# Optimization experiments

Measured on AMD Instinct MI355X. Metric: run time of the kernel, lower is better.

The kernel has to match this reference:

```python
import jax, jax.numpy as jnp
import numpy as np

NODE_IN, EDGE_IN, HID, L = 16, 8, 128, 4
N_NODES, N_EDGES = 50000, 600000
EPS = 1e-5


def setup_inputs() -> dict:
    key = jax.random.key(0)
    ks = jax.random.split(key, 20)
    def lin(k, fan_in, fan_out):
        b = 1.0 / np.sqrt(fan_in)
        kw, kb = jax.random.split(k)
        return (jax.random.uniform(kw, (fan_in, fan_out), jnp.float32, -b, b),
                jax.random.uniform(kb, (fan_out,), jnp.float32, -b, b))
    x = jax.random.normal(ks[0], (N_NODES, NODE_IN), jnp.float32)
    edge_index = jax.random.randint(ks[1], (2, N_EDGES), 0, N_NODES, jnp.int64)
    edge_attr = jax.random.normal(ks[2], (N_EDGES, EDGE_IN), jnp.float32)
    node_w, node_b = lin(ks[3], NODE_IN, HID)
    edge_w, edge_b = lin(ks[4], EDGE_IN, HID)
    lnode_w, lnode_b, ledge_w, ledge_b, adm_w, adm_b = [], [], [], [], [], []
    for l in range(L):
        w, b = lin(ks[5 + 3 * l], HID, HID); lnode_w.append(w); lnode_b.append(b)
        w, b = lin(ks[6 + 3 * l], HID, HID); ledge_w.append(w); ledge_b.append(b)
        w, b = lin(ks[7 + 3 * l], HID, 1); adm_w.append(w); adm_b.append(b)
    return {
        "x": x, "edge_index": edge_index, "edge_attr": edge_attr,
        "node_w": node_w, "node_b": node_b, "edge_w": edge_w, "edge_b": edge_b,
        "lnode_w": jnp.stack(lnode_w), "lnode_b": jnp.stack(lnode_b),
        "ledge_w": jnp.stack(ledge_w), "ledge_b": jnp.stack(ledge_b),
        "adm_w": jnp.stack(adm_w), "adm_b": jnp.stack(adm_b),
        "gamma": jnp.ones((L, HID), jnp.float32),
        "beta": jnp.zeros((L, HID), jnp.float32),
    }


def reference(x, edge_index, edge_attr, node_w, node_b, edge_w, edge_b,
              lnode_w, lnode_b, ledge_w, ledge_b, adm_w, adm_b, gamma, beta):
    N = x.shape[0]
    src, dst = edge_index[0], edge_index[1]
    h = x @ node_w + node_b              # [N, HID]
    ea = edge_attr @ edge_w + edge_b     # [E, HID]
    for l in range(lnode_w.shape[0]):
        hn = h @ lnode_w[l] + lnode_b[l]                         # lin_node
        y_mag = jax.nn.sigmoid(ea @ adm_w[l] + adm_b[l])         # [E, 1] admittance gate
        e = ea @ ledge_w[l] + ledge_b[l]                         # lin_edge
        msg = y_mag * (hn[src] + e)                              # gated message [E, HID]
        agg = jax.ops.segment_sum(msg, dst, num_segments=N)      # scatter-add
        mu = jnp.mean(agg, axis=-1, keepdims=True)
        var = jnp.mean((agg - mu) ** 2, axis=-1, keepdims=True)
        xn = (agg - mu) * jax.lax.rsqrt(var + EPS) * gamma[l] + beta[l]
        h = h + jax.nn.relu(xn)          # dropout is identity in eval mode
    return h
```

## Files before the change

kernel.cpp:

```cpp
#include <hip/hip_runtime.h>
#include <math.h>

#define N_NODES 50000
#define N_EDGES 600000
#define HID 128
#define NLAYERS 4
#define NODE_IN 16
#define EDGE_IN 8
#define LN_EPS 1e-5f
#define SCAN_BLOCKS ((N_NODES + 255) / 256)

typedef short bf16x8 __attribute__((ext_vector_type(8)));
typedef float f32x4 __attribute__((ext_vector_type(4)));

__device__ __forceinline__ float b2f(unsigned short u) {
    union { unsigned int i; float f; } v; v.i = ((unsigned int)u) << 16; return v.f;
}
__device__ __forceinline__ unsigned short f2b(float x) {
    union { float f; unsigned int i; } v; v.f = x;
    unsigned int b = v.i + 0x7FFFu + ((v.i >> 16) & 1u);
    return (unsigned short)(b >> 16);
}

__global__ void detect_i64(const int* ei, int* flag) {
    __shared__ int nz;
    if (threadIdx.x == 0) nz = 0;
    __syncthreads();
    int acc = 0;
    for (int i = threadIdx.x; i < 1024; i += blockDim.x)
        if (ei[2 * i + 1] != 0) acc = 1;
    if (acc) atomicOr(&nz, 1);
    __syncthreads();
    if (threadIdx.x == 0) *flag = (nz == 0) ? 1 : 0;
}

__device__ __forceinline__ int edge_src(const void* ei, int f, int e) {
    if (f) return (int)((const long long*)ei)[e];
    return ((const int*)ei)[e];
}
__device__ __forceinline__ int edge_dst(const void* ei, int f, int e) {
    if (f) return (int)((const long long*)ei)[N_EDGES + e];
    return ((const int*)ei)[N_EDGES + e];
}

__global__ void hist_k(const void* ei, const int* flag, int* cursor) {
    int e = blockIdx.x * blockDim.x + threadIdx.x;
    if (e >= N_EDGES) return;
    int f = *flag;
    atomicAdd(&cursor[edge_dst(ei, f, e)], 1);
}

__global__ void scan1_k(const int* __restrict__ cursor, int* __restrict__ locex,
                        int* __restrict__ partials) {
    __shared__ int sd[256];
    int t = threadIdx.x, i = blockIdx.x * 256 + t;
    int v = (i < N_NODES) ? cursor[i] : 0;
    sd[t] = v;
    __syncthreads();
    for (int off = 1; off < 256; off <<= 1) {
        int x = (t >= off) ? sd[t - off] : 0;
        __syncthreads();
        sd[t] += x;
        __syncthreads();
    }
    if (i < N_NODES) locex[i] = sd[t] - v;
    if (t == 255) partials[blockIdx.x] = sd[255];
}

__global__ void scan2_k(int* partials) {
    __shared__ int sd[256];
    int t = threadIdx.x;
    int v = (t < SCAN_BLOCKS) ? partials[t] : 0;
    sd[t] = v;
    __syncthreads();
    for (int off = 1; off < 256; off <<= 1) {
        int x = (t >= off) ? sd[t - off] : 0;
        __syncthreads();
        sd[t] += x;
        __syncthreads();
    }
    if (t < SCAN_BLOCKS) partials[t] = sd[t] - v;
    if (t == 255) partials[SCAN_BLOCKS] = sd[255];
}

__global__ void scan3_k(int* __restrict__ row_ptr, int* __restrict__ cursor,
                        const int* __restrict__ partials) {
    int i = blockIdx.x * 256 + threadIdx.x;
    if (i < N_NODES) {
        int r = row_ptr[i] + partials[blockIdx.x];
        row_ptr[i] = r;
        cursor[i] = r;
    }
    if (i == N_NODES) row_ptr[N_NODES] = partials[SCAN_BLOCKS];
}

__global__ void place_k(const void* ei, const int* flag, int* cursor,
                        int* sorted_src, int* sorted_eid) {
    int e = blockIdx.x * blockDim.x + threadIdx.x;
    if (e >= N_EDGES) return;
    int f = *flag;
    int s = edge_src(ei, f, e);
    int d = edge_dst(ei, f, e);
    int pos = atomicAdd(&cursor[d], 1);
    sorted_src[pos] = s;
    sorted_eid[pos] = e;
}

__global__ void precompute_k(const float* __restrict__ edge_w, const float* __restrict__ edge_b,
                             const float* __restrict__ ledge_w, const float* __restrict__ ledge_b,
                             const float* __restrict__ lnode_b,
                             const float* __restrict__ adm_w, const float* __restrict__ adm_b,
                             float* __restrict__ M, float* __restrict__ cb,
                             float* __restrict__ v, float* __restrict__ cgate) {
    int t = blockIdx.x * 256 + threadIdx.x;
    if (t < 4096) {
        int l = t >> 10, k = (t >> 7) & 7, ch = t & 127;
        const float* lw = ledge_w + (size_t)l * HID * HID;
        float a = 0.f;
        for (int j = 0; j < HID; ++j) a += edge_w[k * HID + j] * lw[j * HID + ch];
        M[t] = a;
    } else if (t < 4608) {
        int u = t - 4096;
        int l = u >> 7, ch = u & 127;
        const float* lw = ledge_w + (size_t)l * HID * HID;
        float a = ledge_b[l * HID + ch] + lnode_b[l * HID + ch];
        for (int j = 0; j < HID; ++j) a += edge_b[j] * lw[j * HID + ch];
        cb[u] = a;
    } else if (t < 4640) {
        int u = t - 4608;
        int l = u >> 3, k = u & 7;
        float a = 0.f;
        for (int j = 0; j < HID; ++j) a += edge_w[k * HID + j] * adm_w[l * HID + j];
        v[u] = a;
    } else if (t < 4644) {
        int l = t - 4640;
        float a = adm_b[l];
        for (int j = 0; j < HID; ++j) a += edge_b[j] * adm_w[l * HID + j];
        cgate[l] = a;
    }
}

__global__ void convertw_k(const float* __restrict__ lnode_w, unsigned short* __restrict__ Wt16) {
    int idx = blockIdx.x * 256 + threadIdx.x;
    if (idx >= NLAYERS * HID * HID) return;
    int l = idx >> 14, r = idx & 16383, n = r >> 7, k = r & 127;
    Wt16[idx] = f2b(lnode_w[(size_t)l * HID * HID + k * HID + n]);
}

__global__ __launch_bounds__(256) void reorder_k(
    const int* __restrict__ sorted_eid, const float* __restrict__ edge_attr,
    const float* __restrict__ vw, const float* __restrict__ cgate,
    float* __restrict__ ea_sorted, float* __restrict__ y_sorted) {
    __shared__ float sv[36];
    if (threadIdx.x < 32) sv[threadIdx.x] = vw[threadIdx.x];
    else if (threadIdx.x < 36) sv[threadIdx.x] = cgate[threadIdx.x - 32];
    __syncthreads();
    int p = blockIdx.x * 256 + threadIdx.x;
    if (p >= N_EDGES) return;
    int eid = sorted_eid[p];
    float4 a0 = ((const float4*)edge_attr)[(size_t)eid * 2];
    float4 a1 = ((const float4*)edge_attr)[(size_t)eid * 2 + 1];
    ((float4*)ea_sorted)[(size_t)p * 2] = a0;
    ((float4*)ea_sorted)[(size_t)p * 2 + 1] = a1;
#pragma unroll
    for (int l = 0; l < NLAYERS; ++l) {
        const float* vl = &sv[l * 8];
        float t = sv[32 + l];
        t += a0.x * vl[0] + a0.y * vl[1] + a0.z * vl[2] + a0.w * vl[3];
        t += a1.x * vl[4] + a1.y * vl[5] + a1.z * vl[6] + a1.w * vl[7];
        y_sorted[(size_t)l * N_EDGES + p] = 1.0f / (1.0f + __expf(-t));
    }
}

__global__ __launch_bounds__(256) void node_stats_k(
    const int* __restrict__ row_ptr, const float* __restrict__ ea_sorted,
    const float* __restrict__ y_sorted,
    float* __restrict__ agg8, float* __restrict__ sy_arr) {
    int lane = threadIdx.x & 63;
    int n = (blockIdx.x * 256 + threadIdx.x) >> 6;
    int es = lane >> 3, k = lane & 7;
    int ps = row_ptr[n], pe = row_ptr[n + 1];
    float a0 = 0.f, a1 = 0.f, a2 = 0.f, a3 = 0.f;
    float s0 = 0.f, s1 = 0.f, s2 = 0.f, s3 = 0.f;
    for (int p = ps + es; p < pe; p += 8) {
        float ea = ea_sorted[(size_t)p * EDGE_IN + k];
        float y0 = y_sorted[(size_t)0 * N_EDGES + p];
        float y1 = y_sorted[(size_t)1 * N_EDGES + p];
        float y2 = y_sorted[(size_t)2 * N_EDGES + p];
        float y3 = y_sorted[(size_t)3 * N_EDGES + p];
        a0 += y0 * ea; a1 += y1 * ea; a2 += y2 * ea; a3 += y3 * ea;
        s0 += y0; s1 += y1; s2 += y2; s3 += y3;
    }
#pragma unroll
    for (int m = 8; m <= 32; m <<= 1) {
        a0 += __shfl_xor(a0, m, 64); a1 += __shfl_xor(a1, m, 64);
        a2 += __shfl_xor(a2, m, 64); a3 += __shfl_xor(a3, m, 64);
        s0 += __shfl_xor(s0, m, 64); s1 += __shfl_xor(s1, m, 64);
        s2 += __shfl_xor(s2, m, 64); s3 += __shfl_xor(s3, m, 64);
    }
    if (lane < 8) {
        agg8[((size_t)0 * N_NODES + n) * 8 + k] = a0;
        agg8[((size_t)1 * N_NODES + n) * 8 + k] = a1;
        agg8[((size_t)2 * N_NODES + n) * 8 + k] = a2;
        agg8[((size_t)3 * N_NODES + n) * 8 + k] = a3;
    }
    if (lane == 0) {
        sy_arr[(size_t)0 * N_NODES + n] = s0;
        sy_arr[(size_t)1 * N_NODES + n] = s1;
        sy_arr[(size_t)2 * N_NODES + n] = s2;
        sy_arr[(size_t)3 * N_NODES + n] = s3;
    }
}

__global__ void node_encode_k(const float* __restrict__ x, const float* __restrict__ nw,
                              const float* __restrict__ nb, float* __restrict__ h,
                              unsigned short* __restrict__ h16) {
    int idx = blockIdx.x * 256 + threadIdx.x;
    if (idx >= N_NODES * HID) return;
    int n = idx >> 7, c = idx & 127;
    float acc = nb[c];
#pragma unroll
    for (int k = 0; k < NODE_IN; ++k) acc += x[n * NODE_IN + k] * nw[k * HID + c];
    h[idx] = acc;
    h16[idx] = f2b(acc);
}

__global__ __launch_bounds__(256) void gather16_k(
    const int* __restrict__ row_ptr, const int* __restrict__ sorted_src,
    const float* __restrict__ y_l, const unsigned short* __restrict__ h16,
    unsigned int* __restrict__ gh16) {
    int lane = threadIdx.x & 63;
    int n = (blockIdx.x * 256 + threadIdx.x) >> 6;
    int ps = row_ptr[n], pe = row_ptr[n + 1];
    float a0 = 0.f, a1 = 0.f;
    int p = ps;
    for (; p + 7 < pe; p += 8) {
        int s[8];
        float y[8];
        unsigned int v[8];
#pragma unroll
        for (int i = 0; i < 8; ++i) { s[i] = sorted_src[p + i]; y[i] = y_l[p + i]; }
#pragma unroll
        for (int i = 0; i < 8; ++i)
            v[i] = *(const unsigned int*)(h16 + (size_t)s[i] * HID + lane * 2);
#pragma unroll
        for (int i = 0; i < 8; ++i) {
            a0 += y[i] * b2f((unsigned short)v[i]);
            a1 += y[i] * b2f((unsigned short)(v[i] >> 16));
        }
    }
    for (; p + 3 < pe; p += 4) {
        int s[4];
        float y[4];
        unsigned int v[4];
#pragma unroll
        for (int i = 0; i < 4; ++i) { s[i] = sorted_src[p + i]; y[i] = y_l[p + i]; }
#pragma unroll
        for (int i = 0; i < 4; ++i)
            v[i] = *(const unsigned int*)(h16 + (size_t)s[i] * HID + lane * 2);
#pragma unroll
        for (int i = 0; i < 4; ++i) {
            a0 += y[i] * b2f((unsigned short)v[i]);
            a1 += y[i] * b2f((unsigned short)(v[i] >> 16));
        }
    }
    for (; p < pe; ++p) {
        float y = y_l[p];
        unsigned int v = *(const unsigned int*)(h16 + (size_t)sorted_src[p] * HID + lane * 2);
        a0 += y * b2f((unsigned short)v);
        a1 += y * b2f((unsigned short)(v >> 16));
    }
    gh16[(size_t)n * 64 + lane] = ((unsigned int)f2b(a1) << 16) | f2b(a0);
}

__global__ __launch_bounds__(256) void mfma_ln_k(
    const unsigned short* __restrict__ gh16, const unsigned short* __restrict__ Wt16,
    const float* __restrict__ M_l, const float* __restrict__ cb_l,
    const float* __restrict__ agg8_l, const float* __restrict__ sy_l,
    const float* __restrict__ gm, const float* __restrict__ bt,
    const float* __restrict__ h_in, float* __restrict__ h_out,
    unsigned short* __restrict__ h16_out) {
    __shared__ float red[4][16][2];
    const int tid = threadIdx.x;
    const int w = tid >> 6, lane = tid & 63;
    const int g = lane >> 4, c = lane & 15;
    const int nbase = blockIdx.x * 16;
    const int cf0 = w * 2;

    bf16x8 afrag[4];
#pragma unroll
    for (int kc = 0; kc < 4; ++kc)
        afrag[kc] = *(const bf16x8*)(gh16 + (size_t)(nbase + c) * HID + kc * 32 + g * 8);

    f32x4 acc[2];
#pragma unroll
    for (int t = 0; t < 2; ++t) {
        acc[t] = (f32x4){0.f, 0.f, 0.f, 0.f};
        const unsigned short* wp = Wt16 + (size_t)((cf0 + t) * 16 + c) * HID + g * 8;
#pragma unroll
        for (int kc = 0; kc < 4; ++kc) {
            bf16x8 bfrag = *(const bf16x8*)(wp + kc * 32);
            acc[t] = __builtin_amdgcn_mfma_f32_16x16x32_bf16(afrag[kc], bfrag, acc[t], 0, 0, 0);
        }
    }

    float cbv[2], gav[2], bev[2], mv[2][8];
#pragma unroll
    for (int t = 0; t < 2; ++t) {
        int ch = (cf0 + t) * 16 + c;
        cbv[t] = cb_l[ch]; gav[t] = gm[ch]; bev[t] = bt[ch];
#pragma unroll
        for (int k = 0; k < 8; ++k) mv[t][k] = M_l[k * HID + ch];
    }
#pragma unroll
    for (int r = 0; r < 4; ++r) {
        int node = nbase + 4 * g + r;
        float sy = sy_l[node];
        float4 t0 = ((const float4*)agg8_l)[(size_t)node * 2];
        float4 t1 = ((const float4*)agg8_l)[(size_t)node * 2 + 1];
        float a8[8] = {t0.x, t0.y, t0.z, t0.w, t1.x, t1.y, t1.z, t1.w};
#pragma unroll
        for (int t = 0; t < 2; ++t) {
            float v = sy * cbv[t];
#pragma unroll
            for (int k = 0; k < 8; ++k) v += a8[k] * mv[t][k];
            acc[t][r] += v;
        }
    }

    float sx[4], sq[4];
#pragma unroll
    for (int r = 0; r < 4; ++r) {
        sx[r] = acc[0][r] + acc[1][r];
        sq[r] = acc[0][r] * acc[0][r] + acc[1][r] * acc[1][r];
    }
#pragma unroll
    for (int m = 1; m <= 8; m <<= 1) {
#pragma unroll
        for (int r = 0; r < 4; ++r) {
            sx[r] += __shfl_xor(sx[r], m, 64);
            sq[r] += __shfl_xor(sq[r], m, 64);
        }
    }
    if (c == 0) {
#pragma unroll
        for (int r = 0; r < 4; ++r) {
            red[w][4 * g + r][0] = sx[r];
            red[w][4 * g + r][1] = sq[r];
        }
    }
    __syncthreads();

#pragma unroll
    for (int r = 0; r < 4; ++r) {
        int row = 4 * g + r;
        float SX = red[0][row][0] + red[1][row][0] + red[2][row][0] + red[3][row][0];
        float SQ = red[0][row][1] + red[1][row][1] + red[2][row][1] + red[3][row][1];
        float mean = SX * (1.0f / HID);
        float var = SQ * (1.0f / HID) - mean * mean;
        float rstd = rsqrtf(var + LN_EPS);
        int node = nbase + row;
#pragma unroll
        for (int t = 0; t < 2; ++t) {
            int ch = (cf0 + t) * 16 + c;
            float d = acc[t][r] - mean;
            float o = h_in[(size_t)node * HID + ch] +
                      fmaxf(d * rstd * gav[t] + bev[t], 0.f);
            h_out[(size_t)node * HID + ch] = o;
            h16_out[(size_t)node * HID + ch] = f2b(o);
        }
    }
}

extern "C" void kernel_launch(void* const* d_in, const int* in_sizes, int n_in,
                              void* d_out, int out_size, void* d_ws, size_t ws_size,
                              hipStream_t stream) {
    const float* x         = (const float*)d_in[0];
    const void*  ei        = d_in[1];
    const float* edge_attr = (const float*)d_in[2];
    const float* node_w    = (const float*)d_in[3];
    const float* node_b    = (const float*)d_in[4];
    const float* edge_w    = (const float*)d_in[5];
    const float* edge_b    = (const float*)d_in[6];
    const float* lnode_w   = (const float*)d_in[7];
    const float* lnode_b   = (const float*)d_in[8];
    const float* ledge_w   = (const float*)d_in[9];
    const float* ledge_b   = (const float*)d_in[10];
    const float* adm_w     = (const float*)d_in[11];
    const float* adm_b     = (const float*)d_in[12];
    const float* gamma     = (const float*)d_in[13];
    const float* beta      = (const float*)d_in[14];
    float* h = (float*)d_out;

    char* wp = (char*)d_ws;
    auto alloc = [&](size_t bytes) -> void* {
        void* p = (void*)wp;
        wp += (bytes + 255) & ~(size_t)255;
        return p;
    };
    int*            flag       = (int*)alloc(256);
    int*            cursor     = (int*)alloc(sizeof(int) * N_NODES);
    int*            row_ptr    = (int*)alloc(sizeof(int) * (N_NODES + 1));
    int*            partials   = (int*)alloc(sizeof(int) * (SCAN_BLOCKS + 1));
    int*            sorted_src = (int*)alloc(sizeof(int) * N_EDGES);
    int*            sorted_eid = (int*)alloc(sizeof(int) * N_EDGES);
    float*          ea_sorted  = (float*)alloc(sizeof(float) * (size_t)N_EDGES * EDGE_IN);
    float*          y_sorted   = (float*)alloc(sizeof(float) * NLAYERS * N_EDGES);
    float*          agg8       = (float*)alloc(sizeof(float) * NLAYERS * N_NODES * 8);
    float*          sy_arr     = (float*)alloc(sizeof(float) * NLAYERS * N_NODES);
    float*          Mw         = (float*)alloc(sizeof(float) * NLAYERS * 8 * HID);
    float*          cbw        = (float*)alloc(sizeof(float) * NLAYERS * HID);
    float*          vw         = (float*)alloc(sizeof(float) * NLAYERS * 8);
    float*          cgate      = (float*)alloc(sizeof(float) * NLAYERS);
    float*          hbuf       = (float*)alloc(sizeof(float) * (size_t)N_NODES * HID);
    unsigned short* h16        = (unsigned short*)alloc(sizeof(short) * (size_t)N_NODES * HID);
    unsigned short* gh16       = (unsigned short*)alloc(sizeof(short) * (size_t)N_NODES * HID);
    unsigned short* Wt16       = (unsigned short*)alloc(sizeof(short) * NLAYERS * HID * HID);
    (void)ws_size; (void)in_sizes; (void)n_in; (void)out_size;

    hipMemsetAsync(cursor, 0, sizeof(int) * N_NODES, stream);
    detect_i64<<<1, 256, 0, stream>>>((const int*)ei, flag);
    hist_k<<<(N_EDGES + 255) / 256, 256, 0, stream>>>(ei, flag, cursor);
    scan1_k<<<SCAN_BLOCKS, 256, 0, stream>>>(cursor, row_ptr, partials);
    scan2_k<<<1, 256, 0, stream>>>(partials);
    scan3_k<<<SCAN_BLOCKS, 256, 0, stream>>>(row_ptr, cursor, partials);
    place_k<<<(N_EDGES + 255) / 256, 256, 0, stream>>>(ei, flag, cursor, sorted_src, sorted_eid);
    precompute_k<<<19, 256, 0, stream>>>(edge_w, edge_b, ledge_w, ledge_b, lnode_b,
                                         adm_w, adm_b, Mw, cbw, vw, cgate);
    convertw_k<<<(NLAYERS * HID * HID + 255) / 256, 256, 0, stream>>>(lnode_w, Wt16);
    reorder_k<<<(N_EDGES + 255) / 256, 256, 0, stream>>>(sorted_eid, edge_attr,
                                                         vw, cgate, ea_sorted, y_sorted);
    node_stats_k<<<N_NODES / 4, 256, 0, stream>>>(row_ptr, ea_sorted, y_sorted,
                                                  agg8, sy_arr);
    node_encode_k<<<(N_NODES * HID + 255) / 256, 256, 0, stream>>>(x, node_w, node_b, h, h16);

    float* hin = h;
    float* hout = hbuf;
    for (int l = 0; l < NLAYERS; ++l) {
        gather16_k<<<N_NODES / 4, 256, 0, stream>>>(
            row_ptr, sorted_src, y_sorted + (size_t)l * N_EDGES, h16, (unsigned int*)gh16);
        mfma_ln_k<<<N_NODES / 16, 256, 0, stream>>>(
            gh16, Wt16 + (size_t)l * HID * HID,
            Mw + (size_t)l * 8 * HID, cbw + (size_t)l * HID,
            agg8 + (size_t)l * N_NODES * 8, sy_arr + (size_t)l * N_NODES,
            gamma + (size_t)l * HID, beta + (size_t)l * HID,
            hin, hout, h16);
        float* t = hin; hin = hout; hout = t;
    }
}
```

Measured before the change: 376.8 us.

## Apply node linear before gather and fuse gather with LayerNorm epilogue

```diff
diff --git a/kernel.cpp b/kernel.cpp
--- a/kernel.cpp
+++ b/kernel.cpp
@@ -225,10 +225,46 @@
     h16[idx] = f2b(acc);
 }
 
-__global__ __launch_bounds__(256) void gather16_k(
+__global__ __launch_bounds__(256) void mfma_hn_k(
+    const unsigned short* __restrict__ h16, const unsigned short* __restrict__ Wt16,
+    unsigned short* __restrict__ hn16) {
+    const int tid = threadIdx.x;
+    const int w = tid >> 6, lane = tid & 63;
+    const int g = lane >> 4, c = lane & 15;
+    const int nbase = blockIdx.x * 16;
+    const int cf0 = w * 2;
+
+    bf16x8 afrag[4];
+#pragma unroll
+    for (int kc = 0; kc < 4; ++kc)
+        afrag[kc] = *(const bf16x8*)(h16 + (size_t)(nbase + c) * HID + kc * 32 + g * 8);
+
+    f32x4 acc[2];
+#pragma unroll
+    for (int t = 0; t < 2; ++t) {
+        acc[t] = (f32x4){0.f, 0.f, 0.f, 0.f};
+        const unsigned short* wp = Wt16 + (size_t)((cf0 + t) * 16 + c) * HID + g * 8;
+#pragma unroll
+        for (int kc = 0; kc < 4; ++kc) {
+            bf16x8 bfrag = *(const bf16x8*)(wp + kc * 32);
+            acc[t] = __builtin_amdgcn_mfma_f32_16x16x32_bf16(afrag[kc], bfrag, acc[t], 0, 0, 0);
+        }
+    }
+#pragma unroll
+    for (int t = 0; t < 2; ++t)
+#pragma unroll
+        for (int r = 0; r < 4; ++r)
+            hn16[(size_t)(nbase + 4 * g + r) * HID + (cf0 + t) * 16 + c] = f2b(acc[t][r]);
+}
+
+__global__ __launch_bounds__(256) void gather_ln_k(
     const int* __restrict__ row_ptr, const int* __restrict__ sorted_src,
-    const float* __restrict__ y_l, const unsigned short* __restrict__ h16,
-    unsigned int* __restrict__ gh16) {
+    const float* __restrict__ y_l, const unsigned short* __restrict__ hn16,
+    const float* __restrict__ M_l, const float* __restrict__ cb_l,
+    const float* __restrict__ agg8_l, const float* __restrict__ sy_l,
+    const float* __restrict__ gm, const float* __restrict__ bt,
+    const float* __restrict__ h_in, float* __restrict__ h_out,
+    unsigned short* __restrict__ h16_out) {
     int lane = threadIdx.x & 63;
     int n = (blockIdx.x * 256 + threadIdx.x) >> 6;
     int ps = row_ptr[n], pe = row_ptr[n + 1];
@@ -242,7 +278,7 @@
         for (int i = 0; i < 8; ++i) { s[i] = sorted_src[p + i]; y[i] = y_l[p + i]; }
 #pragma unroll
         for (int i = 0; i < 8; ++i)
-            v[i] = *(const unsigned int*)(h16 + (size_t)s[i] * HID + lane * 2);
+            v[i] = *(const unsigned int*)(hn16 + (size_t)s[i] * HID + lane * 2);
 #pragma unroll
         for (int i = 0; i < 8; ++i) {
             a0 += y[i] * b2f((unsigned short)v[i]);
@@ -257,7 +293,7 @@
         for (int i = 0; i < 4; ++i) { s[i] = sorted_src[p + i]; y[i] = y_l[p + i]; }
 #pragma unroll
         for (int i = 0; i < 4; ++i)
-            v[i] = *(const unsigned int*)(h16 + (size_t)s[i] * HID + lane * 2);
+            v[i] = *(const unsigned int*)(hn16 + (size_t)s[i] * HID + lane * 2);
 #pragma unroll
         for (int i = 0; i < 4; ++i) {
             a0 += y[i] * b2f((unsigned short)v[i]);
@@ -266,110 +302,45 @@
     }
     for (; p < pe; ++p) {
         float y = y_l[p];
-        unsigned int v = *(const unsigned int*)(h16 + (size_t)sorted_src[p] * HID + lane * 2);
+        unsigned int v = *(const unsigned int*)(hn16 + (size_t)sorted_src[p] * HID + lane * 2);
         a0 += y * b2f((unsigned short)v);
         a1 += y * b2f((unsigned short)(v >> 16));
     }
-    gh16[(size_t)n * 64 + lane] = ((unsigned int)f2b(a1) << 16) | f2b(a0);
-}
-
-__global__ __launch_bounds__(256) void mfma_ln_k(
-    const unsigned short* __restrict__ gh16, const unsigned short* __restrict__ Wt16,
-    const float* __restrict__ M_l, const float* __restrict__ cb_l,
-    const float* __restrict__ agg8_l, const float* __restrict__ sy_l,
-    const float* __restrict__ gm, const float* __restrict__ bt,
-    const float* __restrict__ h_in, float* __restrict__ h_out,
-    unsigned short* __restrict__ h16_out) {
-    __shared__ float red[4][16][2];
-    const int tid = threadIdx.x;
-    const int w = tid >> 6, lane = tid & 63;
-    const int g = lane >> 4, c = lane & 15;
-    const int nbase = blockIdx.x * 16;
-    const int cf0 = w * 2;
-
-    bf16x8 afrag[4];
-#pragma unroll
-    for (int kc = 0; kc < 4; ++kc)
-        afrag[kc] = *(const bf16x8*)(gh16 + (size_t)(nbase + c) * HID + kc * 32 + g * 8);
-
-    f32x4 acc[2];
-#pragma unroll
-    for (int t = 0; t < 2; ++t) {
-        acc[t] = (f32x4){0.f, 0.f, 0.f, 0.f};
-        const unsigned short* wp = Wt16 + (size_t)((cf0 + t) * 16 + c) * HID + g * 8;
-#pragma unroll
-        for (int kc = 0; kc < 4; ++kc) {
-            bf16x8 bfrag = *(const bf16x8*)(wp + kc * 32);
-            acc[t] = __builtin_amdgcn_mfma_f32_16x16x32_bf16(afrag[kc], bfrag, acc[t], 0, 0, 0);
-        }
-    }
-
-    float cbv[2], gav[2], bev[2], mv[2][8];
-#pragma unroll
-    for (int t = 0; t < 2; ++t) {
-        int ch = (cf0 + t) * 16 + c;
-        cbv[t] = cb_l[ch]; gav[t] = gm[ch]; bev[t] = bt[ch];
-#pragma unroll
-        for (int k = 0; k < 8; ++k) mv[t][k] = M_l[k * HID + ch];
-    }
-#pragma unroll
-    for (int r = 0; r < 4; ++r) {
-        int node = nbase + 4 * g + r;
-        float sy = sy_l[node];
-        float4 t0 = ((const float4*)agg8_l)[(size_t)node * 2];
-        float4 t1 = ((const float4*)agg8_l)[(size_t)node * 2 + 1];
-        float a8[8] = {t0.x, t0.y, t0.z, t0.w, t1.x, t1.y, t1.z, t1.w};
-#pragma unroll
-        for (int t = 0; t < 2; ++t) {
-            float v = sy * cbv[t];
-#pragma unroll
-            for (int k = 0; k < 8; ++k) v += a8[k] * mv[t][k];
-            acc[t][r] += v;
-        }
-    }
-
-    float sx[4], sq[4];
-#pragma unroll
-    for (int r = 0; r < 4; ++r) {
-        sx[r] = acc[0][r] + acc[1][r];
-        sq[r] = acc[0][r] * acc[0][r] + acc[1][r] * acc[1][r];
-    }
-#pragma unroll
-    for (int m = 1; m <= 8; m <<= 1) {
-#pragma unroll
-        for (int r = 0; r < 4; ++r) {
-            sx[r] += __shfl_xor(sx[r], m, 64);
-            sq[r] += __shfl_xor(sq[r], m, 64);
-        }
-    }
-    if (c == 0) {
-#pragma unroll
-        for (int r = 0; r < 4; ++r) {
-            red[w][4 * g + r][0] = sx[r];
-            red[w][4 * g + r][1] = sq[r];
-        }
-    }
-    __syncthreads();
-
-#pragma unroll
-    for (int r = 0; r < 4; ++r) {
-        int row = 4 * g + r;
-        float SX = red[0][row][0] + red[1][row][0] + red[2][row][0] + red[3][row][0];
-        float SQ = red[0][row][1] + red[1][row][1] + red[2][row][1] + red[3][row][1];
-        float mean = SX * (1.0f / HID);
-        float var = SQ * (1.0f / HID) - mean * mean;
-        float rstd = rsqrtf(var + LN_EPS);
-        int node = nbase + row;
-#pragma unroll
-        for (int t = 0; t < 2; ++t) {
-            int ch = (cf0 + t) * 16 + c;
-            float d = acc[t][r] - mean;
-            float o = h_in[(size_t)node * HID + ch] +
-                      fmaxf(d * rstd * gav[t] + bev[t], 0.f);
-            h_out[(size_t)node * HID + ch] = o;
-            h16_out[(size_t)node * HID + ch] = f2b(o);
-        }
-    }
+
+    int c0 = lane * 2;
+    float sy = sy_l[n];
+    float4 t0 = ((const float4*)agg8_l)[(size_t)n * 2];
+    float4 t1 = ((const float4*)agg8_l)[(size_t)n * 2 + 1];
+    float a8[8] = {t0.x, t0.y, t0.z, t0.w, t1.x, t1.y, t1.z, t1.w};
+    float2 cb2 = *(const float2*)&cb_l[c0];
+    a0 += sy * cb2.x;
+    a1 += sy * cb2.y;
+#pragma unroll
+    for (int k = 0; k < 8; ++k) {
+        float2 m2 = *(const float2*)&M_l[k * HID + c0];
+        a0 += a8[k] * m2.x;
+        a1 += a8[k] * m2.y;
+    }
+
+    float s = a0 + a1;
+    float q = a0 * a0 + a1 * a1;
+#pragma unroll
+    for (int m = 1; m <= 32; m <<= 1) {
+        s += __shfl_xor(s, m, 64);
+        q += __shfl_xor(q, m, 64);
+    }
+    float mean = s * (1.0f / HID);
+    float var = q * (1.0f / HID) - mean * mean;
+    float rstd = rsqrtf(var + LN_EPS);
+
+    float2 g2 = *(const float2*)&gm[c0];
+    float2 b2 = *(const float2*)&bt[c0];
+    float2 hi = *(const float2*)&h_in[(size_t)n * HID + c0];
+    float o0 = hi.x + fmaxf((a0 - mean) * rstd * g2.x + b2.x, 0.f);
+    float o1 = hi.y + fmaxf((a1 - mean) * rstd * g2.y + b2.y, 0.f);
+    *(float2*)&h_out[(size_t)n * HID + c0] = make_float2(o0, o1);
+    ((unsigned int*)h16_out)[(size_t)n * 64 + lane] =
+        ((unsigned int)f2b(o1) << 16) | f2b(o0);
 }
 
 extern "C" void kernel_launch(void* const* d_in, const int* in_sizes, int n_in,
@@ -414,7 +385,7 @@
     float*          cgate      = (float*)alloc(sizeof(float) * NLAYERS);
     float*          hbuf       = (float*)alloc(sizeof(float) * (size_t)N_NODES * HID);
     unsigned short* h16        = (unsigned short*)alloc(sizeof(short) * (size_t)N_NODES * HID);
-    unsigned short* gh16       = (unsigned short*)alloc(sizeof(short) * (size_t)N_NODES * HID);
+    unsigned short* hn16       = (unsigned short*)alloc(sizeof(short) * (size_t)N_NODES * HID);
     unsigned short* Wt16       = (unsigned short*)alloc(sizeof(short) * NLAYERS * HID * HID);
     (void)ws_size; (void)in_sizes; (void)n_in; (void)out_size;
 
@@ -437,10 +408,10 @@
     float* hin = h;
     float* hout = hbuf;
     for (int l = 0; l < NLAYERS; ++l) {
-        gather16_k<<<N_NODES / 4, 256, 0, stream>>>(
-            row_ptr, sorted_src, y_sorted + (size_t)l * N_EDGES, h16, (unsigned int*)gh16);
-        mfma_ln_k<<<N_NODES / 16, 256, 0, stream>>>(
-            gh16, Wt16 + (size_t)l * HID * HID,
+        mfma_hn_k<<<N_NODES / 16, 256, 0, stream>>>(
+            h16, Wt16 + (size_t)l * HID * HID, hn16);
+        gather_ln_k<<<N_NODES / 4, 256, 0, stream>>>(
+            row_ptr, sorted_src, y_sorted + (size_t)l * N_EDGES, hn16,
             Mw + (size_t)l * 8 * HID, cbw + (size_t)l * HID,
             agg8 + (size_t)l * N_NODES * 8, sy_arr + (size_t)l * N_NODES,
             gamma + (size_t)l * HID, beta + (size_t)l * HID,
```

Result: slower. 414.4 us (+10.0%).
